# Optimization experiments

Measured on AMD Instinct MI355X. Metric: run time of the kernel, lower is better.

Reference implementation:

```python
import jax, jax.numpy as jnp
import numpy as np

B, T, D, H = 4, 2048, 1024, 16
HD = D // H  # head_dim = 64

def setup_inputs() -> dict:
    key = jax.random.key(0)
    k1, k2, k3 = jax.random.split(key, 3)
    scale_in = 1.0 / np.sqrt(D)
    return {
        "x": jax.random.normal(k1, (B, T, D), dtype=jnp.float32),
        "W_qkv": jax.random.normal(k2, (D, 3 * D), dtype=jnp.float32) * scale_in,
        "b_qkv": jnp.zeros((3 * D,), dtype=jnp.float32),
        "W_out": jax.random.normal(k3, (D, D), dtype=jnp.float32) * scale_in,
        "b_out": jnp.zeros((D,), dtype=jnp.float32),
    }

def reference(x, W_qkv, b_qkv, W_out, b_out):
    Bx, Tx, C = x.shape
    qkv = x @ W_qkv + b_qkv                      # [B,T,3D]
    q, k, v = jnp.split(qkv, 3, axis=-1)
    # [B,T,D] -> [B,H,T,hd]
    def to_heads(t):
        return t.reshape(Bx, Tx, H, HD).transpose(0, 2, 1, 3)
    q, k, v = to_heads(q), to_heads(k), to_heads(v)
    scores = jnp.einsum('bhqd,bhkd->bhqk', q, k) / np.sqrt(HD)  # [B,H,T,T]
    causal = jnp.tril(jnp.ones((Tx, Tx), dtype=bool))
    scores = jnp.where(causal, scores, -jnp.inf)
    attn = jax.nn.softmax(scores, axis=-1)       # dropout p=0 -> identity
    out = jnp.einsum('bhqk,bhkd->bhqd', attn, v)  # [B,H,T,hd]
    out = out.transpose(0, 2, 1, 3).reshape(Bx, Tx, C)
    return out @ W_out + b_out
```

## Files before the change

kernel.cpp:

```cpp
#include <hip/hip_runtime.h>
#include <hip/hip_bf16.h>

#define BB 4
#define TT 2048
#define DD 1024
#define HH 16
#define HDIM 64
#define BT (BB*TT)
#define D3 (3*DD)

typedef __attribute__((ext_vector_type(8))) short bf16x8;
typedef __attribute__((ext_vector_type(4))) float f32x4;

#if __has_builtin(__builtin_amdgcn_exp2f)
#define EXP2(x) __builtin_amdgcn_exp2f(x)
#else
#define EXP2(x) exp2f(x)
#endif

__device__ __forceinline__ ushort f2bf(float f) {
  union { float f; uint32_t u; } v; v.f = f;
  uint32_t u = v.u + 0x7FFFu + ((v.u >> 16) & 1u);
  return (ushort)(u >> 16);
}

__device__ __forceinline__ ushort f2bf_hw(float f) {
  __hip_bfloat16 h = __float2bfloat16(f);
  ushort u;
  __builtin_memcpy(&u, &h, 2);
  return u;
}

__device__ __forceinline__ float bf2f(ushort u) {
  union { uint32_t i; float f; } x; x.i = ((uint32_t)u) << 16; return x.f;
}

__device__ __forceinline__ void gload_lds16(const void* g, void* l) {
  __builtin_amdgcn_global_load_lds((const __attribute__((address_space(1))) void*)g,
                                   (__attribute__((address_space(3))) void*)l, 16, 0, 0);
}

__global__ __launch_bounds__(256)
void prep(const float* __restrict__ x, ushort* __restrict__ x_bf,
          const float* __restrict__ Wq, ushort* __restrict__ Wtq,
          const float* __restrict__ Wo, ushort* __restrict__ Wto,
          uint* __restrict__ ctr) {
  __shared__ ushort Tt[64][68];
  const int bid = blockIdx.x;
  const int tid = threadIdx.x;
  if (bid < 2048) {
    if (bid == 0 && tid == 0) *ctr = 0u;
    int i = bid * 256 + tid;
    const int stride = 2048 * 256;
    const int n4 = BT * DD / 4;
    for (; i < n4; i += stride) {
      float4 v = ((const float4*)x)[i];
      ushort4 o;
      o.x = f2bf(v.x); o.y = f2bf(v.y); o.z = f2bf(v.z); o.w = f2bf(v.w);
      ((ushort4*)x_bf)[i] = o;
    }
  } else {
    const int flat = bid - 2048;
    const bool isQ = flat < 48 * 16;
    const int lx = isQ ? flat : flat - 48 * 16;
    const int N = isQ ? D3 : DD;
    const int nb = N / 64;
    const float* W = isQ ? Wq : Wo;
    ushort* Wt = isQ ? Wtq : Wto;
    const int n0 = (lx % nb) * 64;
    const int k0 = (lx / nb) * 64;

    const int r = tid >> 4;
    const int c4 = (tid & 15) * 4;
    #pragma unroll
    for (int i = 0; i < 4; ++i) {
      int row = r + i * 16;
      float4 v = *(const float4*)&W[(size_t)(k0 + row) * N + n0 + c4];
      Tt[c4 + 0][row] = f2bf(v.x);
      Tt[c4 + 1][row] = f2bf(v.y);
      Tt[c4 + 2][row] = f2bf(v.z);
      Tt[c4 + 3][row] = f2bf(v.w);
    }
    __syncthreads();
    #pragma unroll
    for (int i = 0; i < 4; ++i) {
      int row = r + i * 16;
      ushort4 tv = *(const ushort4*)&Tt[row][c4];
      *(ushort4*)&Wt[(size_t)(n0 + row) * 1024 + k0 + c4] = tv;
    }
  }
}

template<bool F32OUT>
__global__ __launch_bounds__(512, 2)
void gemm_8p(const ushort* __restrict__ A, const ushort* __restrict__ Bw,
             const float* __restrict__ bias, void* __restrict__ C, int N) {
  __shared__ __align__(16) short lds[2 * (128 + 256) * 64];

  const int tid = threadIdx.x;
  const int w = tid >> 6;
  const int wm = w >> 2;
  const int wn = w & 3;
  const int lane = tid & 63;
  const int li = lane & 15, g = lane >> 4;
  const int swz = (li & 7) << 4;

  const int bm = blockIdx.y * 128;
  const int bn = blockIdx.x * 256;
  const ushort* Ag = A + (size_t)bm * 1024;
  const ushort* Bg = Bw + (size_t)bn * 1024;

  const int lrow8 = lane >> 3;
  const int chsw = (lane & 7) ^ lrow8;

  f32x4 acc[4][4] = {};

#define STAGE6(t, p) do { \
  const int kk_ = (t) * 64; \
  short* Ad_ = lds + (p) * 24576; \
  short* Bd_ = Ad_ + 8192; \
  _Pragma("unroll") \
  for (int h_ = 0; h_ < 2; ++h_) { \
    const int r_ = h_ * 64 + w * 8; \
    gload_lds16(Ag + (size_t)(r_ + lrow8) * 1024 + kk_ + chsw * 8, Ad_ + r_ * 64); \
  } \
  _Pragma("unroll") \
  for (int j_ = 0; j_ < 4; ++j_) { \
    const int r_ = j_ * 64 + w * 8; \
    gload_lds16(Bg + (size_t)(r_ + lrow8) * 1024 + kk_ + chsw * 8, Bd_ + r_ * 64); \
  } \
} while (0)

  STAGE6(0, 0);
  asm volatile("s_waitcnt vmcnt(0)" ::: "memory");
  __builtin_amdgcn_sched_barrier(0);
  __builtin_amdgcn_s_barrier();

  for (int s = 0; s < 16; ++s) {
    const int cur = s & 1;
    const char* Ab = (const char*)lds + cur * 49152;
    const char* Bb = Ab + 16384;

    if (s + 1 < 16) STAGE6(s + 1, cur ^ 1);

    #pragma unroll
    for (int kh = 0; kh < 2; ++kh) {
      bf16x8 af[4], bf[4];
      #pragma unroll
      for (int mi = 0; mi < 4; ++mi)
        af[mi] = *(const bf16x8*)(Ab + (wm * 64 + mi * 16 + li) * 128 + ((kh * 64 + g * 16) ^ swz));
      #pragma unroll
      for (int ni = 0; ni < 4; ++ni)
        bf[ni] = *(const bf16x8*)(Bb + (wn * 64 + ni * 16 + li) * 128 + ((kh * 64 + g * 16) ^ swz));
      __builtin_amdgcn_s_setprio(1);
      #pragma unroll
      for (int mi = 0; mi < 4; ++mi)
        #pragma unroll
        for (int ni = 0; ni < 4; ++ni)
          acc[mi][ni] = __builtin_amdgcn_mfma_f32_16x16x32_bf16(af[mi], bf[ni], acc[mi][ni], 0, 0, 0);
      __builtin_amdgcn_s_setprio(0);
      if (kh == 0) __builtin_amdgcn_s_barrier();
    }
    asm volatile("s_waitcnt vmcnt(0)" ::: "memory");
    __builtin_amdgcn_sched_barrier(0);
    __builtin_amdgcn_s_barrier();
  }
#undef STAGE6

  #pragma unroll
  for (int ni = 0; ni < 4; ++ni) {
    int col = bn + wn * 64 + ni * 16 + li;
    float bv = bias[col];
    #pragma unroll
    for (int mi = 0; mi < 4; ++mi) {
      int row = bm + wm * 64 + mi * 16 + g * 4;
      #pragma unroll
      for (int r = 0; r < 4; ++r) {
        float v = acc[mi][ni][r] + bv;
        if (F32OUT) ((float*)C)[(size_t)(row + r) * N + col] = v;
        else        ((ushort*)C)[(size_t)(row + r) * N + col] = f2bf_hw(v);
      }
    }
  }
}

#define NITEMS 1024

__global__ __launch_bounds__(256)
void attn_mfma(const ushort* __restrict__ qkv, ushort* __restrict__ out,
               uint* __restrict__ ctr) {
  __shared__ __align__(16) short Ks[2][64 * 64];
  __shared__ __align__(16) short Vt[2][64 * 64];
  __shared__ __align__(16) short Pl[4 * 16 * 64];

  volatile int* s_item = (volatile int*)&Pl[0];

  const int tid = threadIdx.x;
  const int w = tid >> 6;
  const int lane = tid & 63;
  const int li = lane & 15, g = lane >> 4;
  const int sw = (li & 7) << 4;

  char* PlB = (char*)Pl + w * 2048;

  const int krow0 = tid >> 3;
  const int kc = tid & 7;
  const int d0 = (tid >> 5) * 8;
  const int kp = tid & 31;
  const int kswz = (kc * 16) ^ ((krow0 & 7) << 4);

  for (;;) {
    if (tid == 0) *s_item = (int)atomicAdd(ctr, 1u);
    __syncthreads();
    const int item = *s_item;
    __syncthreads();
    if (item >= NITEMS) return;

    const int qt = 15 - (item >> 6);
    const int bh = item & 63;
    const int h = bh & 15, b = bh >> 4;
    const int qg0 = qt * 128 + w * 32;

    bf16x8 qfr[2][2];
    #pragma unroll
    for (int qf = 0; qf < 2; ++qf) {
      const ushort* qrow = qkv + (size_t)(b * TT + qg0 + qf * 16 + li) * D3 + h * HDIM;
      #pragma unroll
      for (int c = 0; c < 2; ++c) {
        uint4 raw = *(const uint4*)(qrow + c * 32 + g * 8);
        const ushort* rp = (const ushort*)&raw;
        bf16x8 v;
        #pragma unroll
        for (int j = 0; j < 8; ++j)
          v[j] = (short)f2bf_hw(bf2f(rp[j]) * 0.18033688f);
        qfr[qf][c] = v;
      }
    }

    f32x4 o[4][2] = {};
    float lsum[2] = {0.f, 0.f};

    const ushort* kbase = qkv + (size_t)b * TT * D3 + DD + h * HDIM;
    const ushort* vbase = kbase + DD;

    const int nw = qt + 1;
    const int itlast = 2 * qt + (w >> 1);

    uint4 kpre0, kpre1, kpre2, kpre3, vpre0, vpre1, vpre2, vpre3;
    {
      const ushort* kg = kbase + (size_t)krow0 * D3 + kc * 8;
      kpre0 = *(const uint4*)kg;
      kpre1 = *(const uint4*)(kg + (size_t)32 * D3);
      kpre2 = *(const uint4*)(kg + (size_t)64 * D3);
      kpre3 = *(const uint4*)(kg + (size_t)96 * D3);
      const ushort* vg = vbase + (size_t)(2 * kp) * D3 + d0;
      vpre0 = *(const uint4*)vg;
      vpre1 = *(const uint4*)(vg + D3);
      vpre2 = *(const uint4*)(vg + (size_t)64 * D3);
      vpre3 = *(const uint4*)(vg + (size_t)65 * D3);
    }

    for (int it = 0; it < nw; ++it) {
      {
        char* Ks0 = (char*)Ks[0];
        char* Ks1 = (char*)Ks[1];
        *(uint4*)(Ks0 + krow0 * 128 + kswz) = kpre0;
        *(uint4*)(Ks0 + (krow0 + 32) * 128 + kswz) = kpre1;
        *(uint4*)(Ks1 + krow0 * 128 + kswz) = kpre2;
        *(uint4*)(Ks1 + (krow0 + 32) * 128 + kswz) = kpre3;
        char* Vt0 = (char*)Vt[0];
        char* Vt1 = (char*)Vt[1];
        const ushort* pa = (const ushort*)&vpre0;
        const ushort* pb = (const ushort*)&vpre1;
        const ushort* pc = (const ushort*)&vpre2;
        const ushort* pd = (const ushort*)&vpre3;
        #pragma unroll
        for (int j = 0; j < 8; ++j) {
          uint32_t pk0 = (uint32_t)pa[j] | ((uint32_t)pb[j] << 16);
          uint32_t pk1 = (uint32_t)pc[j] | ((uint32_t)pd[j] << 16);
          *(uint32_t*)(Vt0 + (d0 + j) * 128 + ((4 * kp) ^ (j << 4))) = pk0;
          *(uint32_t*)(Vt1 + (d0 + j) * 128 + ((4 * kp) ^ (j << 4))) = pk1;
        }
      }
      __syncthreads();
      if (it + 1 < nw) {
        const ushort* kg = kbase + (size_t)((it + 1) * 128 + krow0) * D3 + kc * 8;
        kpre0 = *(const uint4*)kg;
        kpre1 = *(const uint4*)(kg + (size_t)32 * D3);
        kpre2 = *(const uint4*)(kg + (size_t)64 * D3);
        kpre3 = *(const uint4*)(kg + (size_t)96 * D3);
        const ushort* vg = vbase + (size_t)((it + 1) * 128 + 2 * kp) * D3 + d0;
        vpre0 = *(const uint4*)vg;
        vpre1 = *(const uint4*)(vg + D3);
        vpre2 = *(const uint4*)(vg + (size_t)64 * D3);
        vpre3 = *(const uint4*)(vg + (size_t)65 * D3);
      }
      #pragma unroll
      for (int c = 0; c < 2; ++c) {
        const int t = 2 * it + c;
        if (t <= itlast) {
          const bool domask = (t == itlast);
          const int k0 = t * 64;
          const char* KsB = (const char*)Ks[c];
          const char* VtB = (const char*)Vt[c];
          bf16x8 pf[2][2];
          f32x4 s[2][4];
          __builtin_amdgcn_s_setprio(1);
          #pragma unroll
          for (int kt = 0; kt < 4; ++kt) {
            const int row = kt * 16 + li;
            bf16x8 kf0 = *(bf16x8*)(KsB + row * 128 + ((g * 16) ^ sw));
            bf16x8 kf1 = *(bf16x8*)(KsB + row * 128 + ((64 + g * 16) ^ sw));
            #pragma unroll
            for (int qf = 0; qf < 2; ++qf) {
              f32x4 a = {0.f, 0.f, 0.f, 0.f};
              a = __builtin_amdgcn_mfma_f32_16x16x32_bf16(kf0, qfr[qf][0], a, 0, 0, 0);
              a = __builtin_amdgcn_mfma_f32_16x16x32_bf16(kf1, qfr[qf][1], a, 0, 0, 0);
              s[qf][kt] = a;
            }
          }
          __builtin_amdgcn_s_setprio(0);
          #pragma unroll
          for (int qf = 0; qf < 2; ++qf) {
            const int qrow = qg0 + qf * 16 + li;
            if (domask) {
              #pragma unroll
              for (int kt = 0; kt < 4; ++kt)
                #pragma unroll
                for (int r = 0; r < 4; ++r) {
                  int key = k0 + kt * 16 + g * 4 + r;
                  if (key > qrow) s[qf][kt][r] = -1e30f;
                }
            }
            float ls = 0.f;
            #pragma unroll
            for (int kt = 0; kt < 4; ++kt) {
              float p0 = EXP2(s[qf][kt][0]);
              float p1 = EXP2(s[qf][kt][1]);
              float p2 = EXP2(s[qf][kt][2]);
              float p3 = EXP2(s[qf][kt][3]);
              ls += (p0 + p1) + (p2 + p3);
              uint2 val;
              val.x = (uint32_t)f2bf_hw(p0) | ((uint32_t)f2bf_hw(p1) << 16);
              val.y = (uint32_t)f2bf_hw(p2) | ((uint32_t)f2bf_hw(p3) << 16);
              *(uint2*)(PlB + li * 128 + ((kt * 32 + g * 8) ^ sw)) = val;
            }
            lsum[qf] += ls;
            pf[qf][0] = *(bf16x8*)(PlB + li * 128 + ((g * 16) ^ sw));
            pf[qf][1] = *(bf16x8*)(PlB + li * 128 + ((64 + g * 16) ^ sw));
          }
          __builtin_amdgcn_s_setprio(1);
          #pragma unroll
          for (int dt = 0; dt < 4; ++dt) {
            const int vrow = dt * 16 + li;
            bf16x8 vf0 = *(bf16x8*)(VtB + vrow * 128 + ((g * 16) ^ sw));
            bf16x8 vf1 = *(bf16x8*)(VtB + vrow * 128 + ((64 + g * 16) ^ sw));
            #pragma unroll
            for (int qf = 0; qf < 2; ++qf) {
              o[dt][qf] = __builtin_amdgcn_mfma_f32_16x16x32_bf16(vf0, pf[qf][0], o[dt][qf], 0, 0, 0);
              o[dt][qf] = __builtin_amdgcn_mfma_f32_16x16x32_bf16(vf1, pf[qf][1], o[dt][qf], 0, 0, 0);
            }
          }
          __builtin_amdgcn_s_setprio(0);
        }
      }
      __syncthreads();
    }

    #pragma unroll
    for (int qf = 0; qf < 2; ++qf) {
      float lt = lsum[qf];
      lt += __shfl_xor(lt, 16);
      lt += __shfl_xor(lt, 32);
      float inv = 1.f / lt;
      ushort* orow = out + (size_t)(b * TT + qg0 + qf * 16 + li) * DD + h * HDIM;
      #pragma unroll
      for (int dt = 0; dt < 4; ++dt) {
        uint2 pk;
        pk.x = (uint32_t)f2bf_hw(o[dt][qf][0] * inv) | ((uint32_t)f2bf_hw(o[dt][qf][1] * inv) << 16);
        pk.y = (uint32_t)f2bf_hw(o[dt][qf][2] * inv) | ((uint32_t)f2bf_hw(o[dt][qf][3] * inv) << 16);
        *(uint2*)&orow[dt * 16 + g * 4] = pk;
      }
    }
  }
}

extern "C" void kernel_launch(void* const* d_in, const int* in_sizes, int n_in,
                              void* d_out, int out_size, void* d_ws, size_t ws_size,
                              hipStream_t stream) {
  const float* x     = (const float*)d_in[0];
  const float* W_qkv = (const float*)d_in[1];
  const float* b_qkv = (const float*)d_in[2];
  const float* W_out = (const float*)d_in[3];
  const float* b_out = (const float*)d_in[4];
  float* out = (float*)d_out;

  ushort* x_bf   = (ushort*)d_ws;
  ushort* wtq    = x_bf + (size_t)BT * DD;
  ushort* wto    = wtq + (size_t)D3 * DD;
  ushort* qkv_bf = wto + (size_t)DD * DD;
  ushort* att_bf = qkv_bf + (size_t)BT * D3;
  uint*   ctr    = (uint*)(att_bf + (size_t)BT * DD);

  prep<<<dim3(2048 + 48 * 16 + 16 * 16), 256, 0, stream>>>(x, x_bf, W_qkv, wtq, W_out, wto, ctr);

  gemm_8p<false><<<dim3(D3 / 256, BT / 128), 512, 0, stream>>>(x_bf, wtq, b_qkv, (void*)qkv_bf, D3);
  attn_mfma<<<dim3(1024), 256, 0, stream>>>(qkv_bf, att_bf, ctr);
  gemm_8p<true><<<dim3(DD / 256, BT / 128), 512, 0, stream>>>(att_bf, wto, b_out, (void*)out, DD);
}
```

Measured before the change: 178.9 us.

## Enlarge attention query tile to 256 rows with 8 waves sharing K/V

The attention kernel now runs 512-thread blocks with 8 waves, each block covering 256 query rows instead of 128, which halves the number of work items. The first 256 threads stage K tiles and the second 256 stage transposed V tiles, so each thread does half the global loads it did before. Each K/V tile in shared memory now feeds twice as many queries, cutting global and LDS traffic per query. In exchange, the coarser causal work items give the dynamic scheduler less room to balance load across CUs, and the larger blocks may lower occupancy.

```diff
diff --git a/kernel.cpp b/kernel.cpp
--- a/kernel.cpp
+++ b/kernel.cpp
@@ -184,14 +184,14 @@
   }
 }
 
-#define NITEMS 1024
-
-__global__ __launch_bounds__(256)
+#define NITEMS 512
+
+__global__ __launch_bounds__(512)
 void attn_mfma(const ushort* __restrict__ qkv, ushort* __restrict__ out,
                uint* __restrict__ ctr) {
   __shared__ __align__(16) short Ks[2][64 * 64];
   __shared__ __align__(16) short Vt[2][64 * 64];
-  __shared__ __align__(16) short Pl[4 * 16 * 64];
+  __shared__ __align__(16) short Pl[8 * 16 * 64];
 
   volatile int* s_item = (volatile int*)&Pl[0];
 
@@ -203,10 +203,12 @@
 
   char* PlB = (char*)Pl + w * 2048;
 
-  const int krow0 = tid >> 3;
-  const int kc = tid & 7;
-  const int d0 = (tid >> 5) * 8;
-  const int kp = tid & 31;
+  const int st = tid & 255;
+  const bool isK = (tid < 256);
+  const int krow0 = st >> 3;
+  const int kc = st & 7;
+  const int d0 = (st >> 5) * 8;
+  const int kp = st & 31;
   const int kswz = (kc * 16) ^ ((krow0 & 7) << 4);
 
   for (;;) {
@@ -216,10 +218,10 @@
     __syncthreads();
     if (item >= NITEMS) return;
 
-    const int qt = 15 - (item >> 6);
+    const int qt = 7 - (item >> 6);
     const int bh = item & 63;
     const int h = bh & 15, b = bh >> 4;
-    const int qg0 = qt * 128 + w * 32;
+    const int qg0 = qt * 256 + w * 32;
 
     bf16x8 qfr[2][2];
     #pragma unroll
@@ -243,37 +245,39 @@
     const ushort* kbase = qkv + (size_t)b * TT * D3 + DD + h * HDIM;
     const ushort* vbase = kbase + DD;
 
-    const int nw = qt + 1;
-    const int itlast = 2 * qt + (w >> 1);
-
-    uint4 kpre0, kpre1, kpre2, kpre3, vpre0, vpre1, vpre2, vpre3;
-    {
+    const int nw = 2 * (qt + 1);
+    const int itlast = 4 * qt + (w >> 1);
+
+    uint4 pre0, pre1, pre2, pre3;
+    if (isK) {
       const ushort* kg = kbase + (size_t)krow0 * D3 + kc * 8;
-      kpre0 = *(const uint4*)kg;
-      kpre1 = *(const uint4*)(kg + (size_t)32 * D3);
-      kpre2 = *(const uint4*)(kg + (size_t)64 * D3);
-      kpre3 = *(const uint4*)(kg + (size_t)96 * D3);
+      pre0 = *(const uint4*)kg;
+      pre1 = *(const uint4*)(kg + (size_t)32 * D3);
+      pre2 = *(const uint4*)(kg + (size_t)64 * D3);
+      pre3 = *(const uint4*)(kg + (size_t)96 * D3);
+    } else {
       const ushort* vg = vbase + (size_t)(2 * kp) * D3 + d0;
-      vpre0 = *(const uint4*)vg;
-      vpre1 = *(const uint4*)(vg + D3);
-      vpre2 = *(const uint4*)(vg + (size_t)64 * D3);
-      vpre3 = *(const uint4*)(vg + (size_t)65 * D3);
+      pre0 = *(const uint4*)vg;
+      pre1 = *(const uint4*)(vg + D3);
+      pre2 = *(const uint4*)(vg + (size_t)64 * D3);
+      pre3 = *(const uint4*)(vg + (size_t)65 * D3);
     }
 
     for (int it = 0; it < nw; ++it) {
-      {
+      if (isK) {
         char* Ks0 = (char*)Ks[0];
         char* Ks1 = (char*)Ks[1];
-        *(uint4*)(Ks0 + krow0 * 128 + kswz) = kpre0;
-        *(uint4*)(Ks0 + (krow0 + 32) * 128 + kswz) = kpre1;
-        *(uint4*)(Ks1 + krow0 * 128 + kswz) = kpre2;
-        *(uint4*)(Ks1 + (krow0 + 32) * 128 + kswz) = kpre3;
+        *(uint4*)(Ks0 + krow0 * 128 + kswz) = pre0;
+        *(uint4*)(Ks0 + (krow0 + 32) * 128 + kswz) = pre1;
+        *(uint4*)(Ks1 + krow0 * 128 + kswz) = pre2;
+        *(uint4*)(Ks1 + (krow0 + 32) * 128 + kswz) = pre3;
+      } else {
         char* Vt0 = (char*)Vt[0];
         char* Vt1 = (char*)Vt[1];
-        const ushort* pa = (const ushort*)&vpre0;
-        const ushort* pb = (const ushort*)&vpre1;
-        const ushort* pc = (const ushort*)&vpre2;
-        const ushort* pd = (const ushort*)&vpre3;
+        const ushort* pa = (const ushort*)&pre0;
+        const ushort* pb = (const ushort*)&pre1;
+        const ushort* pc = (const ushort*)&pre2;
+        const ushort* pd = (const ushort*)&pre3;
         #pragma unroll
         for (int j = 0; j < 8; ++j) {
           uint32_t pk0 = (uint32_t)pa[j] | ((uint32_t)pb[j] << 16);
@@ -284,16 +288,19 @@
       }
       __syncthreads();
       if (it + 1 < nw) {
-        const ushort* kg = kbase + (size_t)((it + 1) * 128 + krow0) * D3 + kc * 8;
-        kpre0 = *(const uint4*)kg;
-        kpre1 = *(const uint4*)(kg + (size_t)32 * D3);
-        kpre2 = *(const uint4*)(kg + (size_t)64 * D3);
-        kpre3 = *(const uint4*)(kg + (size_t)96 * D3);
-        const ushort* vg = vbase + (size_t)((it + 1) * 128 + 2 * kp) * D3 + d0;
-        vpre0 = *(const uint4*)vg;
-        vpre1 = *(const uint4*)(vg + D3);
-        vpre2 = *(const uint4*)(vg + (size_t)64 * D3);
-        vpre3 = *(const uint4*)(vg + (size_t)65 * D3);
+        if (isK) {
+          const ushort* kg = kbase + (size_t)((it + 1) * 128 + krow0) * D3 + kc * 8;
+          pre0 = *(const uint4*)kg;
+          pre1 = *(const uint4*)(kg + (size_t)32 * D3);
+          pre2 = *(const uint4*)(kg + (size_t)64 * D3);
+          pre3 = *(const uint4*)(kg + (size_t)96 * D3);
+        } else {
+          const ushort* vg = vbase + (size_t)((it + 1) * 128 + 2 * kp) * D3 + d0;
+          pre0 = *(const uint4*)vg;
+          pre1 = *(const uint4*)(vg + D3);
+          pre2 = *(const uint4*)(vg + (size_t)64 * D3);
+          pre3 = *(const uint4*)(vg + (size_t)65 * D3);
+        }
       }
       #pragma unroll
       for (int c = 0; c < 2; ++c) {
@@ -405,6 +412,6 @@
   prep<<<dim3(2048 + 48 * 16 + 16 * 16), 256, 0, stream>>>(x, x_bf, W_qkv, wtq, W_out, wto, ctr);
 
   gemm_8p<false><<<dim3(D3 / 256, BT / 128), 512, 0, stream>>>(x_bf, wtq, b_qkv, (void*)qkv_bf, D3);
-  attn_mfma<<<dim3(1024), 256, 0, stream>>>(qkv_bf, att_bf, ctr);
+  attn_mfma<<<dim3(512), 512, 0, stream>>>(qkv_bf, att_bf, ctr);
   gemm_8p<true><<<dim3(DD / 256, BT / 128), 512, 0, stream>>>(att_bf, wto, b_out, (void*)out, DD);
 }
```

New measurement: 188.4 us. 1.05x slower.
